# Kernel tuning notes

Measured on AMD Instinct MI355X. Metric: run time of the kernel, lower is better.

The kernel has to match this reference:

```python
import jax, jax.numpy as jnp
import numpy as np

B, C, H, W = 8, 256, 56, 56
K = 3  # kernel size


def _unfold3x3(x):
    """torch nn.Unfold(kernel=3, stride=1, pad=1) -> [B, HW, C*9].

    torch orders the unfolded channel dim as (c, ki, kj) with c slowest.
    """
    b, c, h, w = x.shape
    xp = jnp.pad(x, ((0, 0), (0, 0), (1, 1), (1, 1)))
    # stack 9 shifted views -> [B, C, 9, H, W]
    patches = jnp.stack(
        [xp[:, :, i:i + h, j:j + w] for i in range(K) for j in range(K)],
        axis=2,
    )
    return patches.reshape(b, c * K * K, h * w).transpose(0, 2, 1)


def setup_inputs() -> dict:
    key = jax.random.key(0)
    ks = jax.random.split(key, 8)
    d = C * K * K  # 2304
    s1 = 1.0 / np.sqrt(d)
    s2 = 1.0 / np.sqrt(C)
    return {
        "x": jax.random.normal(ks[0], (B, C, H, W), jnp.float32),
        "W1": jax.random.uniform(ks[1], (d, C), jnp.float32, -s1, s1),
        "b1": jax.random.uniform(ks[2], (C,), jnp.float32, -s1, s1),
        "W2": jax.random.uniform(ks[3], (C, d), jnp.float32, -s2, s2),
        "b2": jax.random.uniform(ks[4], (d,), jnp.float32, -s2, s2),
        "W3": jax.random.uniform(ks[5], (d, C), jnp.float32, -s1, s1),
        "b3": jax.random.uniform(ks[6], (C,), jnp.float32, -s1, s1),
    }


def reference(x, W1, b1, W2, b2, W3, b3):
    t = _unfold3x3(x)                                   # [B, HW, C*9]
    h1 = jax.nn.relu(jnp.einsum('bld,dc->blc', t, W1) + b1)   # [B, HW, C]
    s = jax.nn.sigmoid(jnp.einsum('blc,cd->bld', h1, W2) + b2)  # [B, HW, C*9]
    out = jnp.einsum('bld,dc->blc', t * s, W3) + b3     # [B, HW, C]
    return out
```

## Files before the change

### kernel.cpp

```cpp
#include <hip/hip_runtime.h>

typedef unsigned short u16;
typedef unsigned int u32;
typedef __attribute__((ext_vector_type(8))) short bfrag_t;
typedef __attribute__((ext_vector_type(4))) float accfrag_t;
typedef __attribute__((ext_vector_type(4))) u32 u32x4;

__device__ __forceinline__ u16 f2b(float f) {
    u32 u = __float_as_uint(f);
    u32 r = (u + 0x7FFFu + ((u >> 16) & 1u)) >> 16;
    return (u16)r;
}
__device__ __forceinline__ u32 pkbf16(float lo, float hi) {
    u32 r;
    asm("v_cvt_pk_bf16_f32 %0, %1, %2" : "=v"(r) : "v"(lo), "v"(hi));
    return r;
}
__device__ __forceinline__ float blo(u32 v) { return __uint_as_float(v << 16); }
__device__ __forceinline__ float bhi(u32 v) { return __uint_as_float(v & 0xffff0000u); }

__device__ __forceinline__ void load16(const u16* g, u16* l) {
    __builtin_amdgcn_global_load_lds(
        (__attribute__((address_space(1))) void*)(u16*)g,
        (__attribute__((address_space(3))) void*)l,
        16, 0, 0);
}

__global__ __launch_bounds__(256) void k_prep(
    const float* __restrict__ x, const float* __restrict__ W1,
    const float* __restrict__ W2, const float* __restrict__ W3,
    const float* __restrict__ b2, u16* __restrict__ xtp,
    u16* __restrict__ W1f, u16* __restrict__ W2f,
    u16* __restrict__ W3f, float* __restrict__ b2p) {
    __shared__ __align__(16) char smem[29184];
    const int bid = blockIdx.x;
    const int tid = threadIdx.x;
    if (bid < 928) {
        const int b = bid / 116;
        const int r = bid - b * 116;
        const int hp = r >> 1;
        const int ch = r & 1;
        u16* rowbase = xtp + (size_t)(b * 58 + hp) * 58 * 256;
        if (hp == 0 || hp == 57) {
            if (ch == 0) {
                u32* p = (u32*)rowbase;
                for (int i = tid; i < 58 * 128; i += 256) p[i] = 0;
            }
            return;
        }
        float* lds = (float*)smem;
        const int h = hp - 1;
        const int c0 = ch * 128;
        const float* xb = x + (size_t)(b * 256 + c0) * 3136 + h * 56;
#pragma unroll
        for (int it = 0; it < 7; ++it) {
            const int idx = it * 256 + tid;
            const int cl = idx / 14;
            const int f4 = idx - cl * 14;
            const float4 v = *(const float4*)(xb + (size_t)cl * 3136 + f4 * 4);
            float* d = lds + cl * 57 + f4 * 4;
            d[0] = v.x; d[1] = v.y; d[2] = v.z; d[3] = v.w;
        }
        __syncthreads();
        u32* orow = (u32*)rowbase;
        const int cp = tid & 63;
        const int wg = tid >> 6;
        const float* l0p = lds + (2 * cp) * 57;
        const float* l1p = lds + (2 * cp + 1) * 57;
#pragma unroll
        for (int it = 0; it < 15; ++it) {
            const int wp = it * 4 + wg;
            if (wp < 58) {
                u32 val = 0;
                if (wp >= 1 && wp <= 56) val = pkbf16(l0p[wp - 1], l1p[wp - 1]);
                orow[wp * 128 + ch * 64 + cp] = val;
            }
        }
    } else if (bid < 1072) {
        int b = bid - 928;
        const float* in = b < 72 ? W1 : W3;
        u16* out = b < 72 ? W1f : W3f;
        if (b >= 72) b -= 72;
        const int rrp = b >> 3;
        const int cg = b & 7;
        u16* lds1 = (u16*)smem;
#pragma unroll
        for (int cc = 0; cc < 32; ++cc) {
            int d = (cg * 32 + cc) * 9 + rrp;
            lds1[cc * 256 + tid] = f2b(in[d * 256 + tid]);
        }
        __syncthreads();
        const int kc72 = rrp * 8 + cg;
#pragma unroll
        for (int s = 0; s < 32; ++s) {
            const int w = s >> 2;
            const int o = (s & 3) * 256 + tid;
            const int e = o & 7;
            const int ln = (o >> 3) & 63;
            const int j = o >> 9;
            const int n = w * 32 + j * 16 + (ln & 15);
            const int q = (ln >> 4) * 8 + e;
            out[(w * 72 + kc72) * 1024 + o] = lds1[q * 256 + n];
        }
    } else if (bid < 1144) {
        const int b = bid - 1072;
        const int rr = b >> 3;
        const int w = b & 7;
        u16* lds2 = (u16*)smem;
#pragma unroll
        for (int s = 0; s < 32; ++s) {
            int li = s * 256 + tid;
            int k = li >> 5, dloc = li & 31;
            lds2[k * 32 + dloc] = f2b(W2[k * 2304 + (w * 32 + dloc) * 9 + rr]);
        }
        __syncthreads();
        u16* ob = W2f + (rr * 8 + w) * 8192;
#pragma unroll
        for (int s = 0; s < 32; ++s) {
            const int o = s * 256 + tid;
            const int e = o & 7;
            const int ln = (o >> 3) & 63;
            const int j = (o >> 9) & 1;
            const int kc = o >> 10;
            const int k = kc * 32 + (ln >> 4) * 8 + e;
            const int dloc = j * 16 + (ln & 15);
            ob[o] = lds2[k * 32 + dloc];
        }
    } else {
        int idx = (bid - 1144) * 256 + tid;
        if (idx < 2304) b2p[idx] = b2[(idx & 255) * 9 + (idx >> 8)];
    }
}

__global__ __launch_bounds__(512, 4) void k_fused(
    const u16* __restrict__ xtp, const u16* __restrict__ W1f,
    const u16* __restrict__ W2f, const u16* __restrict__ W3f,
    const float* __restrict__ b1, const float* __restrict__ b2p,
    const float* __restrict__ b3, float* __restrict__ out) {
    __shared__ __align__(16) u16 As[16384];
    __shared__ __align__(16) u16 Us[16384];

    const int tid = threadIdx.x;
    const int wave = tid >> 6;
    const int lane = tid & 63;
    const int fr = lane & 15;
    const int fq = lane >> 4;
    const int l0 = blockIdx.x * 64;
    const int hi = tid >> 8;

    int roff;
    {
        int l = l0 + ((tid >> 2) & 63);
        int b = l / 3136;
        int rem = l - b * 3136;
        int h = rem / 56;
        int w = rem - h * 56;
        roff = ((b * 58 + h + 1) * 58 + (w + 1)) * 256 + (tid & 3) * 8;
    }
    const int stageOff = (wave & 3) * 512 + lane * 8;
    auto shiftOf = [](int rr) { return ((rr / 3 - 1) * 58 + (rr % 3) - 1) * 256; };
    auto stage = [&](u16* buf, int shift) {
#pragma unroll
        for (int q = 0; q < 4; ++q) {
            const int kc = 2 * q + hi;
            load16(xtp + roff + shift + kc * 32, buf + kc * 2048 + stageOff);
        }
    };

    accfrag_t acc[4][2], accO[4][2];
#pragma unroll
    for (int i = 0; i < 4; ++i)
#pragma unroll
        for (int j = 0; j < 2; ++j) {
            acc[i][j] = (accfrag_t)0.f;
            accO[i][j] = (accfrag_t)0.f;
        }

    const u16* w1p = W1f + wave * 73728 + lane * 8;
    stage(As, shiftOf(0));
    for (int rr = 0; rr < 9; ++rr) {
        u16* cur = (rr & 1) ? Us : As;
        u16* nxt = (rr & 1) ? As : Us;
        __syncthreads();
        if (rr < 8) stage(nxt, shiftOf(rr + 1));
#pragma unroll
        for (int kc = 0; kc < 8; ++kc) {
            bfrag_t bf[2], af[4];
#pragma unroll
            for (int j = 0; j < 2; ++j)
                bf[j] = *(const bfrag_t*)(w1p + ((rr * 8 + kc) * 2 + j) * 512);
#pragma unroll
            for (int i = 0; i < 4; ++i)
                af[i] = *(const bfrag_t*)(cur + kc * 2048 + (i * 16 + fr) * 32 + fq * 8);
#pragma unroll
            for (int i = 0; i < 4; ++i)
#pragma unroll
                for (int j = 0; j < 2; ++j)
                    acc[i][j] = __builtin_amdgcn_mfma_f32_16x16x32_bf16(
                        af[i], bf[j], acc[i][j], 0, 0, 0);
        }
    }
    __syncthreads();
#pragma unroll
    for (int i = 0; i < 4; ++i) {
#pragma unroll
        for (int j = 0; j < 2; ++j) {
            const float bv = b1[wave * 32 + j * 16 + fr];
#pragma unroll
            for (int r = 0; r < 4; ++r) {
                float v = acc[i][j][r] + bv;
                v = v > 0.f ? v : 0.f;
                const float vh = __shfl_down(v, 1);
                if (!(lane & 1))
                    *(u32*)&As[wave * 2048 + (i * 16 + fq * 4 + r) * 32 + j * 16 + fr] =
                        pkbf16(v, vh);
            }
        }
    }
    __syncthreads();

    const u16* w3p = W3f + wave * 73728 + lane * 8;
    for (int rr = 0; rr < 9; ++rr) {
        const int shift = shiftOf(rr);
        u32x4 tvreg[4];
#pragma unroll
        for (int q = 0; q < 4; ++q) {
            const int kc = 2 * q + hi;
            tvreg[q] = *(const u32x4*)(xtp + roff + shift + kc * 32);
        }
#pragma unroll
        for (int i = 0; i < 4; ++i)
#pragma unroll
            for (int j = 0; j < 2; ++j) acc[i][j] = (accfrag_t)0.f;
        const u16* w2p = W2f + (rr * 8 + wave) * 8192 + lane * 8;
#pragma unroll
        for (int kc = 0; kc < 8; ++kc) {
            bfrag_t bf[2], af[4];
#pragma unroll
            for (int j = 0; j < 2; ++j)
                bf[j] = *(const bfrag_t*)(w2p + (kc * 2 + j) * 512);
#pragma unroll
            for (int i = 0; i < 4; ++i)
                af[i] = *(const bfrag_t*)(As + kc * 2048 + (i * 16 + fr) * 32 + fq * 8);
#pragma unroll
            for (int i = 0; i < 4; ++i)
#pragma unroll
                for (int j = 0; j < 2; ++j)
                    acc[i][j] = __builtin_amdgcn_mfma_f32_16x16x32_bf16(
                        af[i], bf[j], acc[i][j], 0, 0, 0);
        }
        __syncthreads();
#pragma unroll
        for (int i = 0; i < 4; ++i) {
#pragma unroll
            for (int j = 0; j < 2; ++j) {
                const float bv = b2p[rr * 256 + wave * 32 + j * 16 + fr];
#pragma unroll
                for (int r = 0; r < 4; ++r) {
                    const float z = acc[i][j][r] + bv;
                    const float s = __builtin_amdgcn_rcpf(1.f + __expf(-z));
                    const float sh = __shfl_down(s, 1);
                    if (!(lane & 1))
                        *(u32*)&Us[wave * 2048 + (i * 16 + fq * 4 + r) * 32 + j * 16 + fr] =
                            pkbf16(s, sh);
                }
            }
        }
        __syncthreads();
#pragma unroll
        for (int q = 0; q < 4; ++q) {
            const int kc = 2 * q + hi;
            const int idx = kc * 2048 + ((tid * 8) & 2047);
            u32x4 sv = *(const u32x4*)(Us + idx);
            u32x4 rv;
#pragma unroll
            for (int e = 0; e < 4; ++e)
                rv[e] = pkbf16(blo(sv[e]) * blo(tvreg[q][e]),
                               bhi(sv[e]) * bhi(tvreg[q][e]));
            *(u32x4*)(Us + idx) = rv;
        }
        __syncthreads();
#pragma unroll
        for (int kc = 0; kc < 8; ++kc) {
            bfrag_t bf[2], af[4];
#pragma unroll
            for (int j = 0; j < 2; ++j)
                bf[j] = *(const bfrag_t*)(w3p + ((rr * 8 + kc) * 2 + j) * 512);
#pragma unroll
            for (int i = 0; i < 4; ++i)
                af[i] = *(const bfrag_t*)(Us + kc * 2048 + (i * 16 + fr) * 32 + fq * 8);
#pragma unroll
            for (int i = 0; i < 4; ++i)
#pragma unroll
                for (int j = 0; j < 2; ++j)
                    accO[i][j] = __builtin_amdgcn_mfma_f32_16x16x32_bf16(
                        af[i], bf[j], accO[i][j], 0, 0, 0);
        }
    }

#pragma unroll
    for (int i = 0; i < 4; ++i) {
#pragma unroll
        for (int j = 0; j < 2; ++j) {
            const int col = wave * 32 + j * 16 + fr;
            const float bv = b3[col];
#pragma unroll
            for (int r = 0; r < 4; ++r) {
                const float v = accO[i][j][r] + bv;
                const float vh = __shfl_down(v, 1);
                if (!(lane & 1)) {
                    float2 st = make_float2(v, vh);
                    *(float2*)(out + (size_t)(l0 + i * 16 + fq * 4 + r) * 256 + col) = st;
                }
            }
        }
    }
}

extern "C" void kernel_launch(void* const* d_in, const int* in_sizes, int n_in,
                              void* d_out, int out_size, void* d_ws, size_t ws_size,
                              hipStream_t stream) {
    const float* x  = (const float*)d_in[0];
    const float* W1 = (const float*)d_in[1];
    const float* b1 = (const float*)d_in[2];
    const float* W2 = (const float*)d_in[3];
    const float* b2 = (const float*)d_in[4];
    const float* W3 = (const float*)d_in[5];
    const float* b3 = (const float*)d_in[6];
    float* out = (float*)d_out;

    char* ws = (char*)d_ws;
    u16* xtp = (u16*)ws;  ws += (size_t)8 * 58 * 58 * 256 * 2;
    u16* W1f = (u16*)ws;  ws += (size_t)589824 * 2;
    u16* W2f = (u16*)ws;  ws += (size_t)589824 * 2;
    u16* W3f = (u16*)ws;  ws += (size_t)589824 * 2;
    float* b2p = (float*)ws;

    k_prep<<<1153, 256, 0, stream>>>(x, W1, W2, W3, b2, xtp, W1f, W2f, W3f, b2p);
    k_fused<<<392, 512, 0, stream>>>(xtp, W1f, W2f, W3f, b1, b2p, b3, out);
}
```

Before: 206.4 us.

## Retile waves to 2x4 grid, swizzle LDS layout, and trim barriers in fused kernel

Reorganises the 8 waves from a 1x8 column split into a 2x4 row/column grid, so each wave computes 32 rows by 64 columns. Each wave now loads half as many A fragments and twice as many B fragments per step. It applies an XOR swizzle to the LDS tile layout for staging, the A-fragment reads and the elementwise writes, to cut bank conflicts. It also moves the t-value global load after the W2 GEMM and drops two __syncthreads per iteration, because each wave now handles only its own LDS region in the elementwise stage. This shifts more weight traffic from global/L2 per wave and depends on the new ownership pattern being race-free.

Measured after the change: 234.8 us. 1.14x slower.

```diff
diff --git a/kernel.cpp b/kernel.cpp
--- a/kernel.cpp
+++ b/kernel.cpp
@@ -145,38 +145,54 @@
     const int lane = tid & 63;
     const int fr = lane & 15;
     const int fq = lane >> 4;
+    const int wr = wave >> 2;
+    const int wc = wave & 3;
     const int l0 = blockIdx.x * 64;
-    const int hi = tid >> 8;
-
-    int roff;
-    {
-        int l = l0 + ((tid >> 2) & 63);
-        int b = l / 3136;
-        int rem = l - b * 3136;
-        int h = rem / 56;
-        int w = rem - h * 56;
-        roff = ((b * 58 + h + 1) * 58 + (w + 1)) * 256 + (tid & 3) * 8;
-    }
-    const int stageOff = (wave & 3) * 512 + lane * 8;
+
+    const int swz = (lane & 3) ^ ((lane >> 3) & 3);
+    int roffs[4], ldst[4];
+#pragma unroll
+    for (int q = 0; q < 4; ++q) {
+        const int row = wr * 32 + (q & 1) * 16 + (lane >> 2);
+        const int l = l0 + row;
+        const int b = l / 3136;
+        const int rem = l - b * 3136;
+        const int h = rem / 56;
+        const int w = rem - h * 56;
+        const int sk = 2 * wc + (q >> 1);
+        roffs[q] = ((b * 58 + h + 1) * 58 + (w + 1)) * 256 + sk * 32 + swz * 8;
+        ldst[q] = sk * 2048 + wr * 1024 + (q & 1) * 512 + lane * 8;
+    }
+    int aoff[2];
+#pragma unroll
+    for (int i = 0; i < 2; ++i)
+        aoff[i] = (wr * 32 + i * 16 + fr) * 32 + ((fq ^ ((fr >> 1) & 3)) * 8);
     auto shiftOf = [](int rr) { return ((rr / 3 - 1) * 58 + (rr % 3) - 1) * 256; };
     auto stage = [&](u16* buf, int shift) {
 #pragma unroll
-        for (int q = 0; q < 4; ++q) {
-            const int kc = 2 * q + hi;
-            load16(xtp + roff + shift + kc * 32, buf + kc * 2048 + stageOff);
-        }
+        for (int q = 0; q < 4; ++q)
+            load16(xtp + roffs[q] + shift, buf + ldst[q]);
     };
-
-    accfrag_t acc[4][2], accO[4][2];
-#pragma unroll
-    for (int i = 0; i < 4; ++i)
-#pragma unroll
-        for (int j = 0; j < 2; ++j) {
+    auto ewidx = [&](int i, int j, int r) {
+        const int row = wr * 32 + i * 16 + fq * 4 + r;
+        const int sk = 2 * wc + (j >> 1);
+        const int sl = ((j & 1) * 2 + (fr >> 3)) ^ ((fq * 2 + (r >> 1)) & 3);
+        return sk * 2048 + row * 32 + sl * 8 + (fr & 7);
+    };
+
+    accfrag_t acc[2][4], accO[2][4];
+#pragma unroll
+    for (int i = 0; i < 2; ++i)
+#pragma unroll
+        for (int j = 0; j < 4; ++j) {
             acc[i][j] = (accfrag_t)0.f;
             accO[i][j] = (accfrag_t)0.f;
         }
 
-    const u16* w1p = W1f + wave * 73728 + lane * 8;
+    const u16* w1p = W1f + (2 * wc) * 73728 + lane * 8;
+    const u16* w3p = W3f + (2 * wc) * 73728 + lane * 8;
+    const u16* w2base = W2f + lane * 8;
+
     stage(As, shiftOf(0));
     for (int rr = 0; rr < 9; ++rr) {
         u16* cur = (rr & 1) ? Us : As;
@@ -185,124 +201,118 @@
         if (rr < 8) stage(nxt, shiftOf(rr + 1));
 #pragma unroll
         for (int kc = 0; kc < 8; ++kc) {
-            bfrag_t bf[2], af[4];
-#pragma unroll
-            for (int j = 0; j < 2; ++j)
-                bf[j] = *(const bfrag_t*)(w1p + ((rr * 8 + kc) * 2 + j) * 512);
-#pragma unroll
-            for (int i = 0; i < 4; ++i)
-                af[i] = *(const bfrag_t*)(cur + kc * 2048 + (i * 16 + fr) * 32 + fq * 8);
-#pragma unroll
-            for (int i = 0; i < 4; ++i)
-#pragma unroll
-                for (int j = 0; j < 2; ++j)
+            bfrag_t bf[4], af[2];
+#pragma unroll
+            for (int j = 0; j < 4; ++j)
+                bf[j] = *(const bfrag_t*)(w1p + (j >> 1) * 73728 +
+                                          ((rr * 8 + kc) * 2 + (j & 1)) * 512);
+#pragma unroll
+            for (int i = 0; i < 2; ++i)
+                af[i] = *(const bfrag_t*)(cur + kc * 2048 + aoff[i]);
+#pragma unroll
+            for (int i = 0; i < 2; ++i)
+#pragma unroll
+                for (int j = 0; j < 4; ++j)
                     acc[i][j] = __builtin_amdgcn_mfma_f32_16x16x32_bf16(
                         af[i], bf[j], acc[i][j], 0, 0, 0);
         }
     }
     __syncthreads();
 #pragma unroll
-    for (int i = 0; i < 4; ++i) {
-#pragma unroll
-        for (int j = 0; j < 2; ++j) {
-            const float bv = b1[wave * 32 + j * 16 + fr];
+    for (int i = 0; i < 2; ++i) {
+#pragma unroll
+        for (int j = 0; j < 4; ++j) {
+            const float bv = b1[wc * 64 + j * 16 + fr];
 #pragma unroll
             for (int r = 0; r < 4; ++r) {
                 float v = acc[i][j][r] + bv;
                 v = v > 0.f ? v : 0.f;
                 const float vh = __shfl_down(v, 1);
                 if (!(lane & 1))
-                    *(u32*)&As[wave * 2048 + (i * 16 + fq * 4 + r) * 32 + j * 16 + fr] =
-                        pkbf16(v, vh);
-            }
-        }
-    }
-    __syncthreads();
-
-    const u16* w3p = W3f + wave * 73728 + lane * 8;
+                    *(u32*)&As[ewidx(i, j, r)] = pkbf16(v, vh);
+            }
+        }
+    }
+
     for (int rr = 0; rr < 9; ++rr) {
+        __syncthreads();
+#pragma unroll
+        for (int i = 0; i < 2; ++i)
+#pragma unroll
+            for (int j = 0; j < 4; ++j) acc[i][j] = (accfrag_t)0.f;
+#pragma unroll
+        for (int kc = 0; kc < 8; ++kc) {
+            bfrag_t bf[4], af[2];
+#pragma unroll
+            for (int j = 0; j < 4; ++j)
+                bf[j] = *(const bfrag_t*)(w2base +
+                        ((rr * 8 + 2 * wc + (j >> 1)) * 8192 +
+                         (kc * 2 + (j & 1)) * 512));
+#pragma unroll
+            for (int i = 0; i < 2; ++i)
+                af[i] = *(const bfrag_t*)(As + kc * 2048 + aoff[i]);
+#pragma unroll
+            for (int i = 0; i < 2; ++i)
+#pragma unroll
+                for (int j = 0; j < 4; ++j)
+                    acc[i][j] = __builtin_amdgcn_mfma_f32_16x16x32_bf16(
+                        af[i], bf[j], acc[i][j], 0, 0, 0);
+        }
         const int shift = shiftOf(rr);
         u32x4 tvreg[4];
 #pragma unroll
-        for (int q = 0; q < 4; ++q) {
-            const int kc = 2 * q + hi;
-            tvreg[q] = *(const u32x4*)(xtp + roff + shift + kc * 32);
-        }
-#pragma unroll
-        for (int i = 0; i < 4; ++i)
-#pragma unroll
-            for (int j = 0; j < 2; ++j) acc[i][j] = (accfrag_t)0.f;
-        const u16* w2p = W2f + (rr * 8 + wave) * 8192 + lane * 8;
-#pragma unroll
-        for (int kc = 0; kc < 8; ++kc) {
-            bfrag_t bf[2], af[4];
-#pragma unroll
-            for (int j = 0; j < 2; ++j)
-                bf[j] = *(const bfrag_t*)(w2p + (kc * 2 + j) * 512);
-#pragma unroll
-            for (int i = 0; i < 4; ++i)
-                af[i] = *(const bfrag_t*)(As + kc * 2048 + (i * 16 + fr) * 32 + fq * 8);
-#pragma unroll
-            for (int i = 0; i < 4; ++i)
-#pragma unroll
-                for (int j = 0; j < 2; ++j)
-                    acc[i][j] = __builtin_amdgcn_mfma_f32_16x16x32_bf16(
-                        af[i], bf[j], acc[i][j], 0, 0, 0);
-        }
-        __syncthreads();
-#pragma unroll
-        for (int i = 0; i < 4; ++i) {
-#pragma unroll
-            for (int j = 0; j < 2; ++j) {
-                const float bv = b2p[rr * 256 + wave * 32 + j * 16 + fr];
+        for (int q = 0; q < 4; ++q)
+            tvreg[q] = *(const u32x4*)(xtp + roffs[q] + shift);
+#pragma unroll
+        for (int i = 0; i < 2; ++i) {
+#pragma unroll
+            for (int j = 0; j < 4; ++j) {
+                const float bv = b2p[rr * 256 + wc * 64 + j * 16 + fr];
 #pragma unroll
                 for (int r = 0; r < 4; ++r) {
                     const float z = acc[i][j][r] + bv;
                     const float s = __builtin_amdgcn_rcpf(1.f + __expf(-z));
                     const float sh = __shfl_down(s, 1);
                     if (!(lane & 1))
-                        *(u32*)&Us[wave * 2048 + (i * 16 + fq * 4 + r) * 32 + j * 16 + fr] =
-                            pkbf16(s, sh);
+                        *(u32*)&Us[ewidx(i, j, r)] = pkbf16(s, sh);
                 }
             }
         }
-        __syncthreads();
 #pragma unroll
         for (int q = 0; q < 4; ++q) {
-            const int kc = 2 * q + hi;
-            const int idx = kc * 2048 + ((tid * 8) & 2047);
-            u32x4 sv = *(const u32x4*)(Us + idx);
+            u32x4 sv = *(const u32x4*)(Us + ldst[q]);
             u32x4 rv;
 #pragma unroll
             for (int e = 0; e < 4; ++e)
                 rv[e] = pkbf16(blo(sv[e]) * blo(tvreg[q][e]),
                                bhi(sv[e]) * bhi(tvreg[q][e]));
-            *(u32x4*)(Us + idx) = rv;
+            *(u32x4*)(Us + ldst[q]) = rv;
         }
         __syncthreads();
 #pragma unroll
         for (int kc = 0; kc < 8; ++kc) {
-            bfrag_t bf[2], af[4];
-#pragma unroll
-            for (int j = 0; j < 2; ++j)
-                bf[j] = *(const bfrag_t*)(w3p + ((rr * 8 + kc) * 2 + j) * 512);
-#pragma unroll
-            for (int i = 0; i < 4; ++i)
-                af[i] = *(const bfrag_t*)(Us + kc * 2048 + (i * 16 + fr) * 32 + fq * 8);
-#pragma unroll
-            for (int i = 0; i < 4; ++i)
-#pragma unroll
-                for (int j = 0; j < 2; ++j)
+            bfrag_t bf[4], af[2];
+#pragma unroll
+            for (int j = 0; j < 4; ++j)
+                bf[j] = *(const bfrag_t*)(w3p + (j >> 1) * 73728 +
+                                          ((rr * 8 + kc) * 2 + (j & 1)) * 512);
+#pragma unroll
+            for (int i = 0; i < 2; ++i)
+                af[i] = *(const bfrag_t*)(Us + kc * 2048 + aoff[i]);
+#pragma unroll
+            for (int i = 0; i < 2; ++i)
+#pragma unroll
+                for (int j = 0; j < 4; ++j)
                     accO[i][j] = __builtin_amdgcn_mfma_f32_16x16x32_bf16(
                         af[i], bf[j], accO[i][j], 0, 0, 0);
         }
     }
 
 #pragma unroll
-    for (int i = 0; i < 4; ++i) {
-#pragma unroll
-        for (int j = 0; j < 2; ++j) {
-            const int col = wave * 32 + j * 16 + fr;
+    for (int i = 0; i < 2; ++i) {
+#pragma unroll
+        for (int j = 0; j < 4; ++j) {
+            const int col = wc * 64 + j * 16 + fr;
             const float bv = b3[col];
 #pragma unroll
             for (int r = 0; r < 4; ++r) {
@@ -310,7 +320,7 @@
                 const float vh = __shfl_down(v, 1);
                 if (!(lane & 1)) {
                     float2 st = make_float2(v, vh);
-                    *(float2*)(out + (size_t)(l0 + i * 16 + fq * 4 + r) * 256 + col) = st;
+                    *(float2*)(out + (size_t)(l0 + wr * 32 + i * 16 + fq * 4 + r) * 256 + col) = st;
                 }
             }
         }
```
